# Kernel tuning notes

Hardware: AMD Instinct MI355X
Metric: run time of the kernel (lower is better)

Reference implementation:

```python
import jax, jax.numpy as jnp
import numpy as np

EMBED = 1024
HEADS = 16
HEAD_DIM = EMBED // HEADS
LN_EPS = 1e-5


def _layer_norm(x, g, b):
    m = jnp.mean(x, axis=-1, keepdims=True)
    v = jnp.mean((x - m) ** 2, axis=-1, keepdims=True)
    return (x - m) / jnp.sqrt(v + LN_EPS) * g + b


def _rope(x):
    # x: (b, H, n, D); standard rotary: freqs repeated (cat(freqs, freqs)), rotate_half
    D = x.shape[-1]
    n = x.shape[2]
    inv_freq = 1.0 / (10000.0 ** (jnp.arange(0, D, 2, dtype=jnp.float32) / D))
    freqs = jnp.arange(n, dtype=jnp.float32)[:, None] * inv_freq[None, :]  # (n, D/2)
    emb = jnp.concatenate([freqs, freqs], axis=-1)  # (n, D)
    cos, sin = jnp.cos(emb), jnp.sin(emb)
    rot = jnp.concatenate([-x[..., D // 2:], x[..., : D // 2]], axis=-1)
    return x * cos + rot * sin


def setup_inputs() -> dict:
    key = jax.random.key(0)
    ks = jax.random.split(key, 8)
    E = EMBED
    s_in = 1.0 / np.sqrt(E)
    return {
        "x": jax.random.normal(ks[0], (2, 2048, E), dtype=jnp.float32),
        "in_proj_w": jax.random.uniform(ks[1], (3 * E, E), jnp.float32, -s_in, s_in),
        "in_proj_b": jnp.zeros((3 * E,), jnp.float32),
        "out_proj_w": jax.random.uniform(ks[2], (E, E), jnp.float32, -s_in, s_in),
        "out_proj_b": jnp.zeros((E,), jnp.float32),
        "geglu_w": jax.random.uniform(ks[3], (2 * E, E), jnp.float32, -s_in, s_in),
        "geglu_b": jnp.zeros((2 * E,), jnp.float32),
        "ln1_g": jnp.ones((E,), jnp.float32),
        "ln1_b": jnp.zeros((E,), jnp.float32),
        "ln2_g": jnp.ones((E,), jnp.float32),
        "ln2_b": jnp.zeros((E,), jnp.float32),
    }


def reference(x, in_proj_w, in_proj_b, out_proj_w, out_proj_b,
              geglu_w, geglu_b, ln1_g, ln1_b, ln2_g, ln2_b):
    b, n, E = x.shape
    H, D = HEADS, HEAD_DIM

    # RoPE applied to raw x (q = k = v = x in the module)
    xh = x.reshape(b, n, H, D).transpose(0, 2, 1, 3)  # (b,H,n,D)
    qr = _rope(xh)
    kr = qr  # q and k are identical pre-projection
    q = qr.transpose(0, 2, 1, 3).reshape(b, n, E)
    k = kr.transpose(0, 2, 1, 3).reshape(b, n, E)
    v = x

    # MultiheadAttention (batch-first semantics): in-proj, per-head SDPA, out-proj
    w_q, w_k, w_v = jnp.split(in_proj_w, 3, axis=0)
    b_q, b_k, b_v = jnp.split(in_proj_b, 3, axis=0)
    qp = (q @ w_q.T + b_q).reshape(b, n, H, D).transpose(0, 2, 1, 3)
    kp = (k @ w_k.T + b_k).reshape(b, n, H, D).transpose(0, 2, 1, 3)
    vp = (v @ w_v.T + b_v).reshape(b, n, H, D).transpose(0, 2, 1, 3)
    scores = jnp.einsum("bhqd,bhkd->bhqk", qp, kp) / jnp.sqrt(jnp.float32(D))
    attn = jax.nn.softmax(scores, axis=-1)
    ctx = jnp.einsum("bhqk,bhkd->bhqd", attn, vp)
    ctx = ctx.transpose(0, 2, 1, 3).reshape(b, n, E)
    attn_out = ctx @ out_proj_w.T + out_proj_b

    # residual + LN1
    h = _layer_norm(x + attn_out, ln1_g, ln1_b)

    # GeGLU: Linear(E -> 2E), chunk, value * gelu(gate) (exact erf gelu like torch)
    proj = h @ geglu_w.T + geglu_b
    val, gate = jnp.split(proj, 2, axis=-1)
    fc_out = val * jax.nn.gelu(gate, approximate=False)

    # residual + LN2
    return _layer_norm(h + fc_out, ln2_g, ln2_b)
```

## Files before the change

### kernel.cpp

```cpp
#include <hip/hip_runtime.h>


typedef __bf16 bf16;
typedef bf16 bf16x8 __attribute__((ext_vector_type(8)));
typedef bf16 bf16x4 __attribute__((ext_vector_type(4)));
typedef float f32x4 __attribute__((ext_vector_type(4)));
typedef float f32x16 __attribute__((ext_vector_type(16)));

#define EMB 1024
#define SEQ 2048
#define NTOK 4096
#define NH 16
#define HD 64

__device__ __forceinline__ f32x4 mfma16(bf16x8 a, bf16x8 b, f32x4 c) {
  return __builtin_amdgcn_mfma_f32_16x16x32_bf16(a, b, c, 0, 0, 0);
}
__device__ __forceinline__ f32x16 mfma32(bf16x8 a, bf16x8 b, f32x16 c) {
  return __builtin_amdgcn_mfma_f32_32x32x16_bf16(a, b, c, 0, 0, 0);
}

__device__ __forceinline__ void gll16(const void* g, void* l) {
  __builtin_amdgcn_global_load_lds(
      (const __attribute__((address_space(1))) void*)g,
      (__attribute__((address_space(3))) void*)l, 16, 0, 0);
}

__device__ __forceinline__ unsigned pk2(float a, float b) {
  union { bf16 h[2]; unsigned u; } t;
  t.h[0] = (bf16)a; t.h[1] = (bf16)b;
  return t.u;
}

__global__ __launch_bounds__(256) void prep_all(
    const float* __restrict__ x, bf16* __restrict__ xb, bf16* __restrict__ qr,
    const float* __restrict__ w0, const float* __restrict__ w1,
    const float* __restrict__ w2, bf16* __restrict__ o0,
    bf16* __restrict__ o1, bf16* __restrict__ o2) {
  const int bid = blockIdx.x;
  if (bid < 8192) {
    int idx = bid * 256 + threadIdx.x;
    int row = idx >> 9;
    int i = idx & 511;
    int h = i >> 5, d2 = i & 31;
    int pos = row & (SEQ - 1);
    int c0 = h * HD + d2;
    size_t base = (size_t)row * EMB;
    float x0 = x[base + c0], x1 = x[base + c0 + 32];
    float invf = exp2f(-(float)d2 * 0.4152410118609203f);
    float ang = (float)pos * invf;
    float sn, cs;
    sincosf(ang, &sn, &cs);
    qr[base + c0] = (bf16)(x0 * cs - x1 * sn);
    qr[base + c0 + 32] = (bf16)(x1 * cs + x0 * sn);
    xb[base + c0] = (bf16)x0;
    xb[base + c0 + 32] = (bf16)x1;
  } else {
    int i = ((bid - 8192) * 256 + threadIdx.x) * 4;
    const float* s; bf16* d; int off;
    if (i < 3 * 1024 * 1024) { s = w0; d = o0; off = i; }
    else if (i < 4 * 1024 * 1024) { s = w1; d = o1; off = i - 3 * 1024 * 1024; }
    else { s = w2; d = o2; off = i - 4 * 1024 * 1024; }
    float4 f = *(const float4*)(s + off);
    d[off] = (bf16)f.x; d[off + 1] = (bf16)f.y;
    d[off + 2] = (bf16)f.z; d[off + 3] = (bf16)f.w;
  }
}

__global__ __launch_bounds__(256) void gemm_in(
    const bf16* __restrict__ Aq, const bf16* __restrict__ Ax,
    const bf16* __restrict__ W, const float* __restrict__ bias,
    bf16* __restrict__ qb, bf16* __restrict__ kv) {
  __shared__ bf16 As[128 * 32];
  __shared__ bf16 Bs[128 * 32];
  const int tid = threadIdx.x, lane = tid & 63, wave = tid >> 6;
  const int quad = lane >> 4, l16 = lane & 15;
  const int m0 = blockIdx.y * 128, n0 = blockIdx.x * 128;
  const bf16* A = (n0 < 2048) ? Aq : Ax;
  const int K = 1024;
  const int wm = (wave >> 1) * 64, wn = (wave & 1) * 64;
  const int srow = wave * 32 + (lane >> 2);
  const int scol = (lane & 3) * 8;
  f32x4 acc[4][4] = {};
  for (int k0 = 0; k0 < K; k0 += 32) {
    __syncthreads();
    gll16(A + (size_t)(m0 + srow) * K + k0 + scol, As + wave * 1024);
    gll16(A + (size_t)(m0 + srow + 16) * K + k0 + scol, As + wave * 1024 + 512);
    gll16(W + (size_t)(n0 + srow) * K + k0 + scol, Bs + wave * 1024);
    gll16(W + (size_t)(n0 + srow + 16) * K + k0 + scol, Bs + wave * 1024 + 512);
    __syncthreads();
    bf16x8 af[4], bw[4];
#pragma unroll
    for (int t = 0; t < 4; ++t) {
      af[t] = *(const bf16x8*)(As + (wm + t * 16 + l16) * 32 + quad * 8);
      bw[t] = *(const bf16x8*)(Bs + (wn + t * 16 + l16) * 32 + quad * 8);
    }
#pragma unroll
    for (int mt = 0; mt < 4; ++mt)
#pragma unroll
      for (int nt = 0; nt < 4; ++nt)
        acc[mt][nt] = mfma16(af[mt], bw[nt], acc[mt][nt]);
  }
  if (n0 < 1024) {
#pragma unroll
    for (int mt = 0; mt < 4; ++mt)
      for (int nt = 0; nt < 4; ++nt) {
        const int n = n0 + wn + nt * 16 + l16;
        const float bv = bias[n];
#pragma unroll
        for (int r = 0; r < 4; ++r) {
          const int m = m0 + wm + mt * 16 + quad * 4 + r;
          qb[(size_t)m * 1024 + n] = (bf16)((acc[mt][nt][r] + bv) * 0.125f);
        }
      }
  } else if (n0 < 2048) {
#pragma unroll
    for (int mt = 0; mt < 4; ++mt)
      for (int nt = 0; nt < 4; ++nt) {
        const int n = n0 + wn + nt * 16 + l16;
        const float bv = bias[n];
        const int kd = n - 1024, hh = kd >> 6, d = kd & 63;
        const int dc = d >> 3, dl = d & 7;
#pragma unroll
        for (int r = 0; r < 4; ++r) {
          const int m = m0 + wm + mt * 16 + quad * 4 + r;
          const int bb = m >> 11, s = m & 2047;
          const int t = s >> 6, kr = s & 63;
          const size_t base = ((size_t)((bb * 16 + hh) * 32 + t)) * 8192;
          kv[base + kr * 64 + ((dc ^ (kr & 7)) << 3) + dl] =
              (bf16)((acc[mt][nt][r] + bv) * 1.4426950408889634f);
        }
      }
  } else {
#pragma unroll
    for (int mt = 0; mt < 4; ++mt)
      for (int nt = 0; nt < 4; ++nt) {
        const int n = n0 + wn + nt * 16 + l16;
        const float bv = bias[n];
        const int vd = n - 2048, hh = vd >> 6, d = vd & 63;
        const int m = m0 + wm + mt * 16 + quad * 4;
        const int bb = m >> 11, s = m & 2047;
        const int t = s >> 6, kt = s & 63;
        const int g = kt >> 4, w = kt & 15;
        const int c = 2 * g + ((w >> 2) & 1);
        const int slot = (w & 8) ? 4 : 0;
        const size_t base = ((size_t)((bb * 16 + hh) * 32 + t)) * 8192 + 4096;
        bf16x4 pkv;
#pragma unroll
        for (int r = 0; r < 4; ++r) pkv[r] = (bf16)(acc[mt][nt][r] + bv);
        *(bf16x4*)(kv + base + d * 64 + ((c ^ (d & 7)) << 3) + slot) = pkv;
      }
  }
}

__global__ __launch_bounds__(256) void gemm_bt(
    const bf16* __restrict__ A, const bf16* __restrict__ W,
    const float* __restrict__ bias,
    float* __restrict__ outF, bf16* __restrict__ outB,
    int M, int N, int K) {
  __shared__ bf16 As[128 * 32];
  __shared__ bf16 Bs[128 * 32];
  const int tid = threadIdx.x, lane = tid & 63, wave = tid >> 6;
  const int quad = lane >> 4, l16 = lane & 15;
  const int m0 = blockIdx.y * 128, n0 = blockIdx.x * 128;
  const int wm = (wave >> 1) * 64, wn = (wave & 1) * 64;
  const int srow = wave * 32 + (lane >> 2);
  const int scol = (lane & 3) * 8;
  f32x4 acc[4][4] = {};
  for (int k0 = 0; k0 < K; k0 += 32) {
    __syncthreads();
    gll16(A + (size_t)(m0 + srow) * K + k0 + scol, As + wave * 1024);
    gll16(A + (size_t)(m0 + srow + 16) * K + k0 + scol, As + wave * 1024 + 512);
    gll16(W + (size_t)(n0 + srow) * K + k0 + scol, Bs + wave * 1024);
    gll16(W + (size_t)(n0 + srow + 16) * K + k0 + scol, Bs + wave * 1024 + 512);
    __syncthreads();
    bf16x8 af[4], bw[4];
#pragma unroll
    for (int t = 0; t < 4; ++t) {
      af[t] = *(const bf16x8*)(As + (wm + t * 16 + l16) * 32 + quad * 8);
      bw[t] = *(const bf16x8*)(Bs + (wn + t * 16 + l16) * 32 + quad * 8);
    }
#pragma unroll
    for (int mt = 0; mt < 4; ++mt)
#pragma unroll
      for (int nt = 0; nt < 4; ++nt)
        acc[mt][nt] = mfma16(af[mt], bw[nt], acc[mt][nt]);
  }
#pragma unroll
  for (int mt = 0; mt < 4; ++mt)
    for (int nt = 0; nt < 4; ++nt) {
      const int n = n0 + wn + nt * 16 + l16;
      const float bv = bias ? bias[n] : 0.0f;
#pragma unroll
      for (int r = 0; r < 4; ++r) {
        const int m = m0 + wm + mt * 16 + quad * 4 + r;
        const float v = acc[mt][nt][r] + bv;
        if (outF) outF[(size_t)m * N + n] = v;
        if (outB) outB[(size_t)m * N + n] = (bf16)v;
      }
    }
}

__global__ __launch_bounds__(256, 2) void attn14(
    const bf16* __restrict__ Q, const bf16* __restrict__ KV,
    bf16* __restrict__ ctx) {
  __shared__ __align__(16) bf16 kvb[2][16384];
  __shared__ float Linv[4][32];
  const int tid = threadIdx.x, lane = tid & 63, wave = tid >> 6;
  const int hi = lane >> 5, l31 = lane & 31, l7 = lane & 7;
  const int bid = blockIdx.x;
  const int hb = (bid & 7) * 4 + ((bid >> 3) & 3);
  const int qt = bid >> 5;
  const int h = hb & 15, b = hb >> 4;

  bf16x8 qf[4];
  {
    const int qrow = qt * 128 + wave * 32 + l31;
    const bf16* qp = Q + (size_t)(b * SEQ + qrow) * 1024 + h * HD + hi * 8;
#pragma unroll
    for (int t = 0; t < 4; ++t) qf[t] = *(const bf16x8*)(qp + t * 16);
  }
  asm volatile("s_waitcnt vmcnt(0)" ::: "memory");

  const int soff = tid * 8;
  const bf16* kvg = KV + ((size_t)(b * NH + h) * 32) * 8192 + soff;
#pragma unroll
  for (int i = 0; i < 8; ++i)
    gll16(kvg + i * 2048, kvb[0] + soff + i * 2048);
#pragma unroll
  for (int i = 0; i < 8; ++i)
    gll16(kvg + 16384 + i * 2048, kvb[1] + soff + i * 2048);

  f32x16 o0 = {}, o1 = {};
  float lpart = 0.0f;
  const f32x16 zf = {};

  for (int t = 0; t < 16; ++t) {
    if (t < 15) asm volatile("s_waitcnt vmcnt(8)" ::: "memory");
    else        asm volatile("s_waitcnt vmcnt(0)" ::: "memory");
    __builtin_amdgcn_s_barrier();
    __builtin_amdgcn_sched_barrier(0);
    const bf16* tb = kvb[t & 1];
#pragma unroll
    for (int half = 0; half < 2; ++half) {
      const bf16* ks = tb + half * 8192;
      const bf16* vs = ks + 4096;
      f32x16 s0, s1;
      __builtin_amdgcn_s_setprio(1);
      {
        const int swc = (hi ^ l7) * 8;
        bf16x8 k0 = *(const bf16x8*)(ks + l31 * 64 + swc);
        bf16x8 k1 = *(const bf16x8*)(ks + (32 + l31) * 64 + swc);
        s0 = mfma32(k0, qf[0], zf);
        s1 = mfma32(k1, qf[0], zf);
      }
#pragma unroll
      for (int tt = 1; tt < 4; ++tt) {
        const int swc = ((tt * 2 + hi) ^ l7) * 8;
        bf16x8 k0 = *(const bf16x8*)(ks + l31 * 64 + swc);
        bf16x8 k1 = *(const bf16x8*)(ks + (32 + l31) * 64 + swc);
        s0 = mfma32(k0, qf[tt], s0);
        s1 = mfma32(k1, qf[tt], s1);
      }
      __builtin_amdgcn_s_setprio(0);
      unsigned u[16];
#pragma unroll
      for (int g = 0; g < 8; ++g) {
        const int base = (g & 3) * 4;
        float e0, e1, e2, e3;
        if (g < 4) {
          e0 = __builtin_amdgcn_exp2f(s0[base]);
          e1 = __builtin_amdgcn_exp2f(s0[base + 1]);
          e2 = __builtin_amdgcn_exp2f(s0[base + 2]);
          e3 = __builtin_amdgcn_exp2f(s0[base + 3]);
        } else {
          e0 = __builtin_amdgcn_exp2f(s1[base]);
          e1 = __builtin_amdgcn_exp2f(s1[base + 1]);
          e2 = __builtin_amdgcn_exp2f(s1[base + 2]);
          e3 = __builtin_amdgcn_exp2f(s1[base + 3]);
        }
        lpart += (e0 + e1) + (e2 + e3);
        u[g * 2] = pk2(e0, e1);
        u[g * 2 + 1] = pk2(e2, e3);
      }
      __builtin_amdgcn_s_setprio(1);
#pragma unroll
      for (int kk = 0; kk < 4; ++kk) {
        union { unsigned w[4]; bf16x8 v; } fw;
        fw.w[0] = u[4 * kk]; fw.w[1] = u[4 * kk + 1];
        fw.w[2] = u[4 * kk + 2]; fw.w[3] = u[4 * kk + 3];
        const int c16 = (2 * kk + hi) ^ l7;
        bf16x8 v0 = *(const bf16x8*)(vs + l31 * 64 + c16 * 8);
        bf16x8 v1 = *(const bf16x8*)(vs + (32 + l31) * 64 + c16 * 8);
        o0 = mfma32(fw.v, v0, o0);
        o1 = mfma32(fw.v, v1, o1);
      }
      __builtin_amdgcn_s_setprio(0);
    }
    __builtin_amdgcn_sched_barrier(0);
    __builtin_amdgcn_s_barrier();
    __builtin_amdgcn_sched_barrier(0);
    if (t + 2 < 16) {
      const bf16* src = kvg + (size_t)(t + 2) * 16384;
      bf16* dst = kvb[t & 1] + soff;
#pragma unroll
      for (int i = 0; i < 8; ++i) gll16(src + i * 2048, dst + i * 2048);
    }
  }
  float ltot = lpart + __shfl_xor(lpart, 32, 64);
  if (lane < 32) Linv[wave][lane] = 1.0f / ltot;
#pragma unroll
  for (int r = 0; r < 16; ++r) {
    const int qloc = (r & 3) + 8 * (r >> 2) + 4 * hi;
    const float inv = Linv[wave][qloc];
    const int qrow = qt * 128 + wave * 32 + qloc;
    bf16* cp = ctx + (size_t)(b * SEQ + qrow) * EMB + h * HD;
    cp[l31] = (bf16)(o0[r] * inv);
    cp[32 + l31] = (bf16)(o1[r] * inv);
  }
}

__global__ __launch_bounds__(256) void ln1_k(
    const float* __restrict__ x, const float* __restrict__ ao,
    const float* __restrict__ g, const float* __restrict__ bta,
    float* __restrict__ hF, bf16* __restrict__ hB) {
  int row = blockIdx.x, tid = threadIdx.x;
  const float* xr = x + (size_t)row * EMB;
  const float* ar = ao + (size_t)row * EMB;
  float v[4], s = 0.0f, s2 = 0.0f;
#pragma unroll
  for (int i = 0; i < 4; ++i) {
    float t = xr[tid + i * 256] + ar[tid + i * 256];
    v[i] = t; s += t; s2 += t * t;
  }
#pragma unroll
  for (int off = 1; off < 64; off <<= 1) {
    s += __shfl_xor(s, off, 64);
    s2 += __shfl_xor(s2, off, 64);
  }
  __shared__ float red[8];
  int wave = tid >> 6, lane = tid & 63;
  if (lane == 0) { red[wave] = s; red[4 + wave] = s2; }
  __syncthreads();
  s = red[0] + red[1] + red[2] + red[3];
  s2 = red[4] + red[5] + red[6] + red[7];
  float mean = s * (1.0f / EMB);
  float var = s2 * (1.0f / EMB) - mean * mean;
  float inv = rsqrtf(var + 1e-5f);
#pragma unroll
  for (int i = 0; i < 4; ++i) {
    int c = tid + i * 256;
    float t = (v[i] - mean) * inv * g[c] + bta[c];
    hF[(size_t)row * EMB + c] = t;
    hB[(size_t)row * EMB + c] = (bf16)t;
  }
}

__global__ __launch_bounds__(256) void geglu_ln2(
    const float* __restrict__ h, const bf16* __restrict__ proj,
    const float* __restrict__ g, const float* __restrict__ bta,
    float* __restrict__ out) {
  int row = blockIdx.x, tid = threadIdx.x;
  const float* hr = h + (size_t)row * EMB;
  const bf16* pr = proj + (size_t)row * 2048;
  float v[4], s = 0.0f, s2 = 0.0f;
#pragma unroll
  for (int i = 0; i < 4; ++i) {
    int c = tid + i * 256;
    float val = (float)pr[c];
    float gate = (float)pr[1024 + c];
    float ge = 0.5f * gate * (1.0f + erff(gate * 0.70710678f));
    float t = hr[c] + val * ge;
    v[i] = t; s += t; s2 += t * t;
  }
#pragma unroll
  for (int off = 1; off < 64; off <<= 1) {
    s += __shfl_xor(s, off, 64);
    s2 += __shfl_xor(s2, off, 64);
  }
  __shared__ float red[8];
  int wave = tid >> 6, lane = tid & 63;
  if (lane == 0) { red[wave] = s; red[4 + wave] = s2; }
  __syncthreads();
  s = red[0] + red[1] + red[2] + red[3];
  s2 = red[4] + red[5] + red[6] + red[7];
  float mean = s * (1.0f / EMB);
  float var = s2 * (1.0f / EMB) - mean * mean;
  float inv = rsqrtf(var + 1e-5f);
#pragma unroll
  for (int i = 0; i < 4; ++i) {
    int c = tid + i * 256;
    out[(size_t)row * EMB + c] = (v[i] - mean) * inv * g[c] + bta[c];
  }
}

extern "C" void kernel_launch(void* const* d_in, const int* in_sizes, int n_in,
                              void* d_out, int out_size, void* d_ws, size_t ws_size,
                              hipStream_t stream) {
  const float* x = (const float*)d_in[0];
  const float* inW = (const float*)d_in[1];
  const float* inB = (const float*)d_in[2];
  const float* outW = (const float*)d_in[3];
  const float* opB = (const float*)d_in[4];
  const float* ggW = (const float*)d_in[5];
  const float* ggB = (const float*)d_in[6];
  const float* g1 = (const float*)d_in[7];
  const float* b1 = (const float*)d_in[8];
  const float* g2 = (const float*)d_in[9];
  const float* b2 = (const float*)d_in[10];
  float* out = (float*)d_out;
  char* ws = (char*)d_ws;
  const size_t MB = 1ull << 20;
  bf16* xb = (bf16*)(ws);
  bf16* hB = (bf16*)(ws);
  bf16* qr = (bf16*)(ws + 8 * MB);
  bf16* ctx = (bf16*)(ws + 8 * MB);
  bf16* wI = (bf16*)(ws + 16 * MB);
  bf16* wO = (bf16*)(ws + 22 * MB);
  bf16* wG = (bf16*)(ws + 24 * MB);
  bf16* qb = (bf16*)(ws + 28 * MB);
  bf16* kv = (bf16*)(ws + 36 * MB);
  bf16* projB = (bf16*)(ws + 28 * MB);
  float* ao = (float*)(ws + 52 * MB);

  prep_all<<<8192 + 6144, 256, 0, stream>>>(x, xb, qr, inW, outW, ggW,
                                            wI, wO, wG);
  gemm_in<<<dim3(24, 32), 256, 0, stream>>>(qr, xb, wI, inB, qb, kv);
  attn14<<<512, 256, 0, stream>>>(qb, kv, ctx);
  gemm_bt<<<dim3(8, 32), 256, 0, stream>>>(ctx, wO, opB, ao, nullptr,
                                           NTOK, 1024, 1024);
  ln1_k<<<NTOK, 256, 0, stream>>>(x, ao, g1, b1, ao, hB);
  gemm_bt<<<dim3(16, 32), 256, 0, stream>>>(hB, wG, ggB, nullptr, projB,
                                            NTOK, 2048, 1024);
  geglu_ln2<<<NTOK, 256, 0, stream>>>(ao, projB, g2, b2, out);
}
```

Baseline: 274.3 us.

## Double-buffer GEMM LDS loads, add XCD-aware block remap, use 128x64 out-proj tile

The three bf16 GEMMs now double-buffer their LDS tiles. The next K-slice is issued with global_load_lds before computing on the current one, and partial vmcnt waits replace the paired __syncthreads. Workgroups are remapped so consecutive tiles land on the same XCD, which should improve L2 reuse. The out-projection GEMM moves to a new 128x64 tile kernel that launches twice as many blocks for better CU occupancy. The cost is double the LDS per block and reliance on hand-written waitcnt ordering.

```diff
diff --git a/kernel.cpp b/kernel.cpp
--- a/kernel.cpp
+++ b/kernel.cpp
@@ -30,6 +30,13 @@
   union { bf16 h[2]; unsigned u; } t;
   t.h[0] = (bf16)a; t.h[1] = (bf16)b;
   return t.u;
+}
+
+__device__ __forceinline__ void xcd_map(int nx, int nwg, int& bx, int& by) {
+  const int lin = blockIdx.y * nx + blockIdx.x;
+  const int id = (lin & 7) * (nwg >> 3) + (lin >> 3);
+  bx = id % nx;
+  by = id / nx;
 }
 
 __global__ __launch_bounds__(256) void prep_all(
@@ -71,35 +78,54 @@
     const bf16* __restrict__ Aq, const bf16* __restrict__ Ax,
     const bf16* __restrict__ W, const float* __restrict__ bias,
     bf16* __restrict__ qb, bf16* __restrict__ kv) {
-  __shared__ bf16 As[128 * 32];
-  __shared__ bf16 Bs[128 * 32];
+  __shared__ bf16 As[2][4096];
+  __shared__ bf16 Bs[2][4096];
   const int tid = threadIdx.x, lane = tid & 63, wave = tid >> 6;
   const int quad = lane >> 4, l16 = lane & 15;
-  const int m0 = blockIdx.y * 128, n0 = blockIdx.x * 128;
+  int bx, by;
+  xcd_map(24, 24 * 32, bx, by);
+  const int m0 = by * 128, n0 = bx * 128;
   const bf16* A = (n0 < 2048) ? Aq : Ax;
   const int K = 1024;
   const int wm = (wave >> 1) * 64, wn = (wave & 1) * 64;
   const int srow = wave * 32 + (lane >> 2);
   const int scol = (lane & 3) * 8;
+  const bf16* a0 = A + (size_t)(m0 + srow) * K + scol;
+  const bf16* a1 = A + (size_t)(m0 + srow + 16) * K + scol;
+  const bf16* w0p = W + (size_t)(n0 + srow) * K + scol;
+  const bf16* w1p = W + (size_t)(n0 + srow + 16) * K + scol;
+  gll16(a0, As[0] + wave * 1024);
+  gll16(a1, As[0] + wave * 1024 + 512);
+  gll16(w0p, Bs[0] + wave * 1024);
+  gll16(w1p, Bs[0] + wave * 1024 + 512);
   f32x4 acc[4][4] = {};
-  for (int k0 = 0; k0 < K; k0 += 32) {
-    __syncthreads();
-    gll16(A + (size_t)(m0 + srow) * K + k0 + scol, As + wave * 1024);
-    gll16(A + (size_t)(m0 + srow + 16) * K + k0 + scol, As + wave * 1024 + 512);
-    gll16(W + (size_t)(n0 + srow) * K + k0 + scol, Bs + wave * 1024);
-    gll16(W + (size_t)(n0 + srow + 16) * K + k0 + scol, Bs + wave * 1024 + 512);
-    __syncthreads();
+  for (int it = 0; it < 32; ++it) {
+    const int cur = it & 1, nxt = cur ^ 1;
+    if (it + 1 < 32) {
+      const int k1 = (it + 1) * 32;
+      gll16(a0 + k1, As[nxt] + wave * 1024);
+      gll16(a1 + k1, As[nxt] + wave * 1024 + 512);
+      gll16(w0p + k1, Bs[nxt] + wave * 1024);
+      gll16(w1p + k1, Bs[nxt] + wave * 1024 + 512);
+      asm volatile("s_waitcnt vmcnt(4)" ::: "memory");
+    } else {
+      asm volatile("s_waitcnt vmcnt(0)" ::: "memory");
+    }
+    __builtin_amdgcn_s_barrier();
+    __builtin_amdgcn_sched_barrier(0);
     bf16x8 af[4], bw[4];
 #pragma unroll
     for (int t = 0; t < 4; ++t) {
-      af[t] = *(const bf16x8*)(As + (wm + t * 16 + l16) * 32 + quad * 8);
-      bw[t] = *(const bf16x8*)(Bs + (wn + t * 16 + l16) * 32 + quad * 8);
+      af[t] = *(const bf16x8*)(As[cur] + (wm + t * 16 + l16) * 32 + quad * 8);
+      bw[t] = *(const bf16x8*)(Bs[cur] + (wn + t * 16 + l16) * 32 + quad * 8);
     }
 #pragma unroll
     for (int mt = 0; mt < 4; ++mt)
 #pragma unroll
       for (int nt = 0; nt < 4; ++nt)
         acc[mt][nt] = mfma16(af[mt], bw[nt], acc[mt][nt]);
+    __builtin_amdgcn_sched_barrier(0);
+    __builtin_amdgcn_s_barrier();
   }
   if (n0 < 1024) {
 #pragma unroll
@@ -157,34 +183,54 @@
     const bf16* __restrict__ A, const bf16* __restrict__ W,
     const float* __restrict__ bias,
     float* __restrict__ outF, bf16* __restrict__ outB,
-    int M, int N, int K) {
-  __shared__ bf16 As[128 * 32];
-  __shared__ bf16 Bs[128 * 32];
+    int M, int N, int K, int nbx) {
+  __shared__ bf16 As[2][4096];
+  __shared__ bf16 Bs[2][4096];
   const int tid = threadIdx.x, lane = tid & 63, wave = tid >> 6;
   const int quad = lane >> 4, l16 = lane & 15;
-  const int m0 = blockIdx.y * 128, n0 = blockIdx.x * 128;
+  int bx, by;
+  xcd_map(nbx, nbx * 32, bx, by);
+  const int m0 = by * 128, n0 = bx * 128;
   const int wm = (wave >> 1) * 64, wn = (wave & 1) * 64;
   const int srow = wave * 32 + (lane >> 2);
   const int scol = (lane & 3) * 8;
+  const bf16* a0 = A + (size_t)(m0 + srow) * K + scol;
+  const bf16* a1 = A + (size_t)(m0 + srow + 16) * K + scol;
+  const bf16* w0p = W + (size_t)(n0 + srow) * K + scol;
+  const bf16* w1p = W + (size_t)(n0 + srow + 16) * K + scol;
+  gll16(a0, As[0] + wave * 1024);
+  gll16(a1, As[0] + wave * 1024 + 512);
+  gll16(w0p, Bs[0] + wave * 1024);
+  gll16(w1p, Bs[0] + wave * 1024 + 512);
   f32x4 acc[4][4] = {};
-  for (int k0 = 0; k0 < K; k0 += 32) {
-    __syncthreads();
-    gll16(A + (size_t)(m0 + srow) * K + k0 + scol, As + wave * 1024);
-    gll16(A + (size_t)(m0 + srow + 16) * K + k0 + scol, As + wave * 1024 + 512);
-    gll16(W + (size_t)(n0 + srow) * K + k0 + scol, Bs + wave * 1024);
-    gll16(W + (size_t)(n0 + srow + 16) * K + k0 + scol, Bs + wave * 1024 + 512);
-    __syncthreads();
+  const int nit = K >> 5;
+  for (int it = 0; it < nit; ++it) {
+    const int cur = it & 1, nxt = cur ^ 1;
+    if (it + 1 < nit) {
+      const int k1 = (it + 1) * 32;
+      gll16(a0 + k1, As[nxt] + wave * 1024);
+      gll16(a1 + k1, As[nxt] + wave * 1024 + 512);
+      gll16(w0p + k1, Bs[nxt] + wave * 1024);
+      gll16(w1p + k1, Bs[nxt] + wave * 1024 + 512);
+      asm volatile("s_waitcnt vmcnt(4)" ::: "memory");
+    } else {
+      asm volatile("s_waitcnt vmcnt(0)" ::: "memory");
+    }
+    __builtin_amdgcn_s_barrier();
+    __builtin_amdgcn_sched_barrier(0);
     bf16x8 af[4], bw[4];
 #pragma unroll
     for (int t = 0; t < 4; ++t) {
-      af[t] = *(const bf16x8*)(As + (wm + t * 16 + l16) * 32 + quad * 8);
-      bw[t] = *(const bf16x8*)(Bs + (wn + t * 16 + l16) * 32 + quad * 8);
+      af[t] = *(const bf16x8*)(As[cur] + (wm + t * 16 + l16) * 32 + quad * 8);
+      bw[t] = *(const bf16x8*)(Bs[cur] + (wn + t * 16 + l16) * 32 + quad * 8);
     }
 #pragma unroll
     for (int mt = 0; mt < 4; ++mt)
 #pragma unroll
       for (int nt = 0; nt < 4; ++nt)
         acc[mt][nt] = mfma16(af[mt], bw[nt], acc[mt][nt]);
+    __builtin_amdgcn_sched_barrier(0);
+    __builtin_amdgcn_s_barrier();
   }
 #pragma unroll
   for (int mt = 0; mt < 4; ++mt)
@@ -197,6 +243,70 @@
         const float v = acc[mt][nt][r] + bv;
         if (outF) outF[(size_t)m * N + n] = v;
         if (outB) outB[(size_t)m * N + n] = (bf16)v;
+      }
+    }
+}
+
+__global__ __launch_bounds__(256) void gemm_bt64(
+    const bf16* __restrict__ A, const bf16* __restrict__ W,
+    const float* __restrict__ bias, float* __restrict__ outF,
+    int M, int N, int K) {
+  __shared__ bf16 As[2][4096];
+  __shared__ bf16 Bs[2][2048];
+  const int tid = threadIdx.x, lane = tid & 63, wave = tid >> 6;
+  const int quad = lane >> 4, l16 = lane & 15;
+  int bx, by;
+  xcd_map(16, 16 * 32, bx, by);
+  const int m0 = by * 128, n0 = bx * 64;
+  const int wm = (wave >> 1) * 64, wn = (wave & 1) * 32;
+  const int srow = wave * 32 + (lane >> 2);
+  const int srowB = wave * 16 + (lane >> 2);
+  const int scol = (lane & 3) * 8;
+  const bf16* a0 = A + (size_t)(m0 + srow) * K + scol;
+  const bf16* a1 = A + (size_t)(m0 + srow + 16) * K + scol;
+  const bf16* w0p = W + (size_t)(n0 + srowB) * K + scol;
+  gll16(a0, As[0] + wave * 1024);
+  gll16(a1, As[0] + wave * 1024 + 512);
+  gll16(w0p, Bs[0] + wave * 512);
+  f32x4 acc[4][2] = {};
+  const int nit = K >> 5;
+  for (int it = 0; it < nit; ++it) {
+    const int cur = it & 1, nxt = cur ^ 1;
+    if (it + 1 < nit) {
+      const int k1 = (it + 1) * 32;
+      gll16(a0 + k1, As[nxt] + wave * 1024);
+      gll16(a1 + k1, As[nxt] + wave * 1024 + 512);
+      gll16(w0p + k1, Bs[nxt] + wave * 512);
+      asm volatile("s_waitcnt vmcnt(3)" ::: "memory");
+    } else {
+      asm volatile("s_waitcnt vmcnt(0)" ::: "memory");
+    }
+    __builtin_amdgcn_s_barrier();
+    __builtin_amdgcn_sched_barrier(0);
+    bf16x8 af[4], bw[2];
+#pragma unroll
+    for (int t = 0; t < 4; ++t)
+      af[t] = *(const bf16x8*)(As[cur] + (wm + t * 16 + l16) * 32 + quad * 8);
+#pragma unroll
+    for (int t = 0; t < 2; ++t)
+      bw[t] = *(const bf16x8*)(Bs[cur] + (wn + t * 16 + l16) * 32 + quad * 8);
+#pragma unroll
+    for (int mt = 0; mt < 4; ++mt)
+#pragma unroll
+      for (int nt = 0; nt < 2; ++nt)
+        acc[mt][nt] = mfma16(af[mt], bw[nt], acc[mt][nt]);
+    __builtin_amdgcn_sched_barrier(0);
+    __builtin_amdgcn_s_barrier();
+  }
+#pragma unroll
+  for (int mt = 0; mt < 4; ++mt)
+    for (int nt = 0; nt < 2; ++nt) {
+      const int n = n0 + wn + nt * 16 + l16;
+      const float bv = bias[n];
+#pragma unroll
+      for (int r = 0; r < 4; ++r) {
+        const int m = m0 + wm + mt * 16 + quad * 4 + r;
+        outF[(size_t)m * N + n] = acc[mt][nt][r] + bv;
       }
     }
 }
@@ -427,10 +537,10 @@
                                             wI, wO, wG);
   gemm_in<<<dim3(24, 32), 256, 0, stream>>>(qr, xb, wI, inB, qb, kv);
   attn14<<<512, 256, 0, stream>>>(qb, kv, ctx);
-  gemm_bt<<<dim3(8, 32), 256, 0, stream>>>(ctx, wO, opB, ao, nullptr,
-                                           NTOK, 1024, 1024);
+  gemm_bt64<<<dim3(16, 32), 256, 0, stream>>>(ctx, wO, opB, ao,
+                                              NTOK, 1024, 1024);
   ln1_k<<<NTOK, 256, 0, stream>>>(x, ao, g1, b1, ao, hB);
   gemm_bt<<<dim3(16, 32), 256, 0, stream>>>(hB, wG, ggB, nullptr, projB,
-                                            NTOK, 2048, 1024);
+                                            NTOK, 2048, 1024, 16);
   geglu_ln2<<<NTOK, 256, 0, stream>>>(ao, projB, g2, b2, out);
 }
```

Result: faster. 268.4 us (-2.1%).
